# Kernel optimization log

Hardware: AMD Instinct MI355X
Metric: run time of the kernel (lower is better)

The kernel has to match this reference:

```python
import jax, jax.numpy as jnp
import numpy as np

B, S, H, D = 8, 1024, 16, 64  # batch, seq, heads, d_heads; hidden = H*D = 1024

def setup_inputs() -> dict:
    key = jax.random.key(0)
    ks = jax.random.split(key, 7)
    sc = 1.0 / np.sqrt(D)
    return {
        "sequences": jax.random.normal(ks[0], (B, S, H * D), dtype=jnp.float32),
        "Wq": jax.random.normal(ks[1], (H, D, D), dtype=jnp.float32) * sc,
        "bq": jax.random.normal(ks[2], (H, D), dtype=jnp.float32) * 0.01,
        "Wk": jax.random.normal(ks[3], (H, D, D), dtype=jnp.float32) * sc,
        "bk": jax.random.normal(ks[4], (H, D), dtype=jnp.float32) * 0.01,
        "Wv": jax.random.normal(ks[5], (H, D, D), dtype=jnp.float32) * sc,
        "bv": jax.random.normal(ks[6], (H, D), dtype=jnp.float32) * 0.01,
    }

def reference(sequences, Wq, bq, Wk, bk, Wv, bv):
    # sequences: [B, S, H*D] -> [B, S, H, D] (head h uses slice h*D:(h+1)*D)
    x = sequences.reshape(B, S, H, D)
    # per-head Linear: y = x @ W.T + b  (torch convention)
    q = jnp.einsum("bshd,hed->bshe", x, Wq) + bq
    k = jnp.einsum("bshd,hed->bshe", x, Wk) + bk
    v = jnp.einsum("bshd,hed->bshe", x, Wv) + bv
    scores = jnp.einsum("bqhd,bkhd->bhqk", q, k) / jnp.sqrt(jnp.float32(D))
    attn = jax.nn.softmax(scores, axis=-1)
    out = jnp.einsum("bhqk,bkhd->bqhd", attn, v)  # [B, S, H, D]
    return out.reshape(B, S, H * D)  # hstack over heads == reshape
```

## Files before the change

kernel.cpp:

```cpp
#include <hip/hip_runtime.h>
#include <hip/hip_bf16.h>


typedef __attribute__((ext_vector_type(8))) short short8;
typedef __attribute__((ext_vector_type(4))) float f32x4;
typedef __attribute__((ext_vector_type(16))) float f32x16;
typedef __attribute__((ext_vector_type(2))) unsigned int u32x2;
typedef __attribute__((ext_vector_type(4))) unsigned int u32x4;

#define MFMA16 __builtin_amdgcn_mfma_f32_16x16x32_bf16
#define MFMA32 __builtin_amdgcn_mfma_f32_32x32x16_bf16

#define QSCALE 0.1803368801111204f

__device__ __forceinline__ unsigned cvt_pk(float lo, float hi) {
  unsigned r;
  asm("v_cvt_pk_bf16_f32 %0, %1, %2" : "=v"(r) : "v"(lo), "v"(hi));
  return r;
}
__device__ __forceinline__ void pl32_swap(unsigned &a, unsigned &b) {
  asm("v_permlane32_swap_b32 %0, %1" : "+v"(a), "+v"(b));
}
__device__ __forceinline__ u32x2 pk4(const f32x4 v) {
  return (u32x2){cvt_pk(v[0], v[1]), cvt_pk(v[2], v[3])};
}
__device__ __forceinline__ void pack_cd(const f32x16& p, short8& lo, short8& hi8) {
  unsigned d0 = cvt_pk(p[0],  p[1]);
  unsigned d2 = cvt_pk(p[4],  p[5]);
  pl32_swap(d0, d2);
  unsigned d1 = cvt_pk(p[2],  p[3]);
  unsigned d3 = cvt_pk(p[6],  p[7]);
  pl32_swap(d1, d3);
  u32x4 a = {d0, d1, d2, d3};
  unsigned e0 = cvt_pk(p[8],  p[9]);
  unsigned e2 = cvt_pk(p[12], p[13]);
  pl32_swap(e0, e2);
  unsigned e1 = cvt_pk(p[10], p[11]);
  unsigned e3 = cvt_pk(p[14], p[15]);
  pl32_swap(e1, e3);
  u32x4 b = {e0, e1, e2, e3};
  lo  = __builtin_bit_cast(short8, a);
  hi8 = __builtin_bit_cast(short8, b);
}
__device__ __forceinline__ void lds_barrier() {
  asm volatile("s_waitcnt lgkmcnt(0)" ::: "memory");
  __builtin_amdgcn_s_barrier();
}

__global__ __launch_bounds__(256) void kv_proj_kernel(
    const float* __restrict__ x,
    const float* __restrict__ Wk, const float* __restrict__ bk,
    const float* __restrict__ Wv, const float* __restrict__ bv,
    unsigned short* __restrict__ kv_ws)
{
  __shared__ unsigned short x_lds[64][72];
  __shared__ unsigned short w_lds[2][64][72];

  const int h    = blockIdx.x & 15;
  const int tb   = blockIdx.x >> 4;
  const int tid  = threadIdx.x;
  const int lane = tid & 63;
  const int wv   = tid >> 6;
  const int g    = lane >> 4;
  const int cc   = lane & 15;

  {
    const int i  = tid >> 2;
    const int q4 = tid & 3;
    const float* xs  = x  + (size_t)(tb * 64 + i) * 1024 + h * 64 + q4 * 16;
    const float* wsk = Wk + (size_t)h * 4096 + i * 64 + q4 * 16;
    const float* wsv = Wv + (size_t)h * 4096 + i * 64 + q4 * 16;
#pragma unroll
    for (int it = 0; it < 4; ++it) {
      const int c = q4 * 16 + it * 4;
      *(u32x2*)&x_lds[i][c]    = pk4(*(const f32x4*)(xs  + it * 4));
      *(u32x2*)&w_lds[0][i][c] = pk4(*(const f32x4*)(wsk + it * 4));
      *(u32x2*)&w_lds[1][i][c] = pk4(*(const f32x4*)(wsv + it * 4));
    }
  }
  __syncthreads();

  f32x4 ak[4], av[4];
#pragma unroll
  for (int f = 0; f < 4; ++f) {
    ak[f] = (f32x4){0.f, 0.f, 0.f, 0.f};
    av[f] = (f32x4){0.f, 0.f, 0.f, 0.f};
  }

  const int arow = wv * 16 + cc;
  const int kc   = g * 8;
#pragma unroll
  for (int kk = 0; kk < 2; ++kk) {
    short8 a = *(const short8*)&x_lds[arow][kk * 32 + kc];
#pragma unroll
    for (int f = 0; f < 4; ++f) {
      const int br = f * 16 + cc;
      ak[f] = MFMA16(a, *(const short8*)&w_lds[0][br][kk * 32 + kc], ak[f], 0, 0, 0);
      av[f] = MFMA16(a, *(const short8*)&w_lds[1][br][kk * 32 + kc], av[f], 0, 0, 0);
    }
  }

  const int b   = tb >> 4;
  const int tk0 = wv * 16 + g * 4;
  unsigned short* kvt = kv_ws + (size_t)(b * 16 + h) * 131072
                              + (size_t)(tb & 15) * 8192;

  __syncthreads();
  unsigned short* Ak = &w_lds[0][0][0];
  unsigned short* Av = &x_lds[0][0];

#pragma unroll
  for (int f = 0; f < 4; ++f) {
    const int e = f * 16 + cc;
    const float bkv = bk[h * 64 + e];
    const float bvv = bv[h * 64 + e];
    u32x2 pkk;
    pkk[0] = cvt_pk(ak[f][0] + bkv, ak[f][1] + bkv);
    pkk[1] = cvt_pk(ak[f][2] + bkv, ak[f][3] + bkv);
    Ak[(tk0 + 0) * 72 + e] = (unsigned short)pkk[0];
    Ak[(tk0 + 1) * 72 + e] = (unsigned short)(pkk[0] >> 16);
    Ak[(tk0 + 2) * 72 + e] = (unsigned short)pkk[1];
    Ak[(tk0 + 3) * 72 + e] = (unsigned short)(pkk[1] >> 16);
    f32x4 vv;
#pragma unroll
    for (int r = 0; r < 4; ++r) vv[r] = av[f][r] + bvv;
    *(u32x2*)&Av[e * 72 + tk0] = pk4(vv);
  }
  __syncthreads();

#pragma unroll
  for (int half = 0; half < 2; ++half) {
    const int c   = tid + half * 256;
    const int oct = c >> 6;
    const int r2  = c & 63;
    const int slot = (oct >> 1) * 128 + (r2 >> 5) * 64 + (oct & 1) * 32 + (r2 & 31);
    short8 kcnk = *(const short8*)&Ak[r2 * 72 + oct * 8];
    *(short8*)&kvt[slot * 8] = kcnk;
    short8 vcnk = *(const short8*)&Av[r2 * 72 + oct * 8];
    *(short8*)&kvt[4096 + slot * 8] = vcnk;
  }
}

__global__ __launch_bounds__(512, 4) void attn_kernel(
    const float* __restrict__ x,
    const float* __restrict__ Wq, const float* __restrict__ bq,
    const unsigned short* __restrict__ kv_ws,
    float* __restrict__ out)
{
  __shared__ __align__(16) char lds[32768];

  const int logical = (blockIdx.x & 7) * 64 + (blockIdx.x >> 3);
  const int qt = logical & 3;
  const int bh = logical >> 2;
  const int b  = bh >> 4;
  const int h  = bh & 15;
  const unsigned short* kvb = kv_ws + (size_t)bh * 131072;

  const int tid = threadIdx.x;
  const int w   = tid >> 6;
  const int l   = tid & 63;
  const int hi  = l >> 5;
  const int cc  = l & 31;

  const unsigned short* sgp = kvb + tid * 8;
  char* wbp = lds + tid * 16;

  short8 st[2];
#pragma unroll
  for (int j = 0; j < 2; ++j) st[j] = *(const short8*)(sgp + j * 4096);

  unsigned short* wq_l = (unsigned short*)lds;
  unsigned short* xh_l = (unsigned short*)(lds + 9216);

  {
    const int r = tid >> 3, s = tid & 7;
    const float* ws = Wq + h * 4096 + r * 64 + s * 8;
    f32x4 v0 = *(const f32x4*)ws;
    f32x4 v1 = *(const f32x4*)(ws + 4);
    u32x4 d = {cvt_pk(v0[0], v0[1]), cvt_pk(v0[2], v0[3]),
               cvt_pk(v1[0], v1[1]), cvt_pk(v1[2], v1[3])};
    *(u32x4*)&wq_l[r * 72 + s * 8] = d;
  }

  short8 qf[4];
  f32x16 qa0 = {}, qa1 = {};
#pragma unroll
  for (int p = 0; p < 2; ++p) {
    {
      const int r = tid >> 2, s = tid & 3;
      const float* xs = x + ((size_t)(b * 1024 + qt * 256 + p * 128 + r)) * 1024
                          + h * 64 + s * 16;
      f32x4 v0 = *(const f32x4*)xs;
      f32x4 v1 = *(const f32x4*)(xs + 4);
      f32x4 v2 = *(const f32x4*)(xs + 8);
      f32x4 v3 = *(const f32x4*)(xs + 12);
      u32x4 d0 = {cvt_pk(v0[0], v0[1]), cvt_pk(v0[2], v0[3]),
                  cvt_pk(v1[0], v1[1]), cvt_pk(v1[2], v1[3])};
      u32x4 d1 = {cvt_pk(v2[0], v2[1]), cvt_pk(v2[2], v2[3]),
                  cvt_pk(v3[0], v3[1]), cvt_pk(v3[2], v3[3])};
      *(u32x4*)&xh_l[r * 72 + s * 16]     = d0;
      *(u32x4*)&xh_l[r * 72 + s * 16 + 8] = d1;
    }
    lds_barrier();
    if ((w >> 2) == p) {
      const int tl = (w & 3) * 32 + cc;
#pragma unroll
      for (int c = 0; c < 4; ++c) {
        short8 xf  = *(const short8*)&xh_l[tl * 72 + c * 16 + hi * 8];
        short8 alo = *(const short8*)&wq_l[cc * 72 + c * 16 + hi * 8];
        short8 ahi = *(const short8*)&wq_l[(32 + cc) * 72 + c * 16 + hi * 8];
        qa0 = MFMA32(alo, xf, qa0, 0, 0, 0);
        qa1 = MFMA32(ahi, xf, qa1, 0, 0, 0);
      }
    }
    lds_barrier();
  }
  {
#pragma unroll
    for (int r = 0; r < 16; ++r) {
      const int e = (r & 3) + 8 * (r >> 2) + 4 * hi;
      qa0[r] = (qa0[r] + bq[h * 64 + e]) * QSCALE;
      qa1[r] = (qa1[r] + bq[h * 64 + 32 + e]) * QSCALE;
    }
    pack_cd(qa0, qf[0], qf[1]);
    pack_cd(qa1, qf[2], qf[3]);
  }

#pragma unroll
  for (int j = 0; j < 2; ++j) *(short8*)(wbp + j * 8192) = st[j];
#pragma unroll
  for (int j = 0; j < 2; ++j) st[j] = *(const short8*)(sgp + 8192 + j * 4096);
  lds_barrier();

  f32x16 ot0 = {}; f32x16 ot1 = {};
  float lsum = 0.f;

  for (int kv = 0; kv < 16; ++kv) {
    if (kv < 15) {
      char* d = wbp + ((kv + 1) & 1) * 16384;
#pragma unroll
      for (int j = 0; j < 2; ++j) *(short8*)(d + j * 8192) = st[j];
      if (kv < 14) {
        const unsigned short* s = sgp + (size_t)(kv + 2) * 8192;
#pragma unroll
        for (int j = 0; j < 2; ++j) st[j] = *(const short8*)(s + j * 4096);
      }
    }
    const char* kb_ = lds + (kv & 1) * 16384;
    const char* vb_ = kb_ + 8192;

    f32x16 s0 = {}; f32x16 s1 = {};
    __builtin_amdgcn_s_setprio(1);
#pragma unroll
    for (int c = 0; c < 4; ++c) {
      s0 = MFMA32(*(const short8*)(kb_ + (c * 128 + l) * 16),      qf[c], s0, 0, 0, 0);
      s1 = MFMA32(*(const short8*)(kb_ + (c * 128 + 64 + l) * 16), qf[c], s1, 0, 0, 0);
    }
    __builtin_amdgcn_s_setprio(0);

    float ps0 = 0.f, ps1 = 0.f;
#pragma unroll
    for (int i = 0; i < 16; ++i) { s0[i] = __builtin_amdgcn_exp2f(s0[i]); ps0 += s0[i]; }
#pragma unroll
    for (int i = 0; i < 16; ++i) { s1[i] = __builtin_amdgcn_exp2f(s1[i]); ps1 += s1[i]; }
    lsum += ps0 + ps1;

#pragma unroll
    for (int kb = 0; kb < 2; ++kb) {
      short8 pa0, pa1;
      pack_cd(kb ? s1 : s0, pa0, pa1);

      const int c20 = kb * 2, c21 = kb * 2 + 1;
      __builtin_amdgcn_s_setprio(1);
      ot0 = MFMA32(*(const short8*)(vb_ + (c20 * 128 + l) * 16),      pa0, ot0, 0, 0, 0);
      ot1 = MFMA32(*(const short8*)(vb_ + (c20 * 128 + 64 + l) * 16), pa0, ot1, 0, 0, 0);
      ot0 = MFMA32(*(const short8*)(vb_ + (c21 * 128 + l) * 16),      pa1, ot0, 0, 0, 0);
      ot1 = MFMA32(*(const short8*)(vb_ + (c21 * 128 + 64 + l) * 16), pa1, ot1, 0, 0, 0);
      __builtin_amdgcn_s_setprio(0);
    }
    lds_barrier();
  }

  const float lt  = lsum + __shfl_xor(lsum, 32, 64);
  const float inv = 1.0f / lt;
  const int s_row = qt * 256 + w * 32 + cc;
  float* op = out + ((size_t)(b * 1024 + s_row) << 10) + h * 64;
#pragma unroll
  for (int rg = 0; rg < 4; ++rg) {
    const int d0 = 8 * rg + 4 * hi;
    f32x4 v0, v1;
#pragma unroll
    for (int j = 0; j < 4; ++j) {
      v0[j] = ot0[rg * 4 + j] * inv;
      v1[j] = ot1[rg * 4 + j] * inv;
    }
    *(f32x4*)(op + d0)      = v0;
    *(f32x4*)(op + 32 + d0) = v1;
  }
}

extern "C" void kernel_launch(void* const* d_in, const int* in_sizes, int n_in,
                              void* d_out, int out_size, void* d_ws, size_t ws_size,
                              hipStream_t stream) {
  const float* x  = (const float*)d_in[0];
  const float* Wq = (const float*)d_in[1];
  const float* bq = (const float*)d_in[2];
  const float* Wk = (const float*)d_in[3];
  const float* bk = (const float*)d_in[4];
  const float* Wv = (const float*)d_in[5];
  const float* bv = (const float*)d_in[6];
  float* out = (float*)d_out;

  unsigned short* kv_ws = (unsigned short*)d_ws;

  kv_proj_kernel<<<2048, 256, 0, stream>>>(x, Wk, bk, Wv, bv, kv_ws);
  attn_kernel<<<512, 512, 0, stream>>>(x, Wq, bq, kv_ws, out);
}
```

Baseline: 70.48 us.

## Compute K/V projection with 32x32 MFMA and write packed layout directly from registers

The K/V projection kernel switches from 16x16x32 MFMAs to 32x32x16 MFMAs. K is computed transposed (W times X) so the accumulator layout matches the attention kernel's expected chunk order. Results are packed with permlane-based pack_cd and stored straight to global memory, removing the LDS staging round-trip and two barriers. This relies on the register-to-slot mapping exactly matching the layout the attention kernel consumes.

Result: no change. 70.56 us (+0.1%).

```diff
diff --git a/kernel.cpp b/kernel.cpp
--- a/kernel.cpp
+++ b/kernel.cpp
@@ -56,13 +56,13 @@
   __shared__ unsigned short x_lds[64][72];
   __shared__ unsigned short w_lds[2][64][72];
 
-  const int h    = blockIdx.x & 15;
-  const int tb   = blockIdx.x >> 4;
-  const int tid  = threadIdx.x;
-  const int lane = tid & 63;
-  const int wv   = tid >> 6;
-  const int g    = lane >> 4;
-  const int cc   = lane & 15;
+  const int h   = blockIdx.x & 15;
+  const int tb  = blockIdx.x >> 4;
+  const int tid = threadIdx.x;
+  const int w   = tid >> 6;
+  const int l   = tid & 63;
+  const int hi  = l >> 5;
+  const int cc  = l & 31;
 
   {
     const int i  = tid >> 2;
@@ -80,64 +80,55 @@
   }
   __syncthreads();
 
-  f32x4 ak[4], av[4];
-#pragma unroll
-  for (int f = 0; f < 4; ++f) {
-    ak[f] = (f32x4){0.f, 0.f, 0.f, 0.f};
-    av[f] = (f32x4){0.f, 0.f, 0.f, 0.f};
-  }
-
-  const int arow = wv * 16 + cc;
-  const int kc   = g * 8;
-#pragma unroll
-  for (int kk = 0; kk < 2; ++kk) {
-    short8 a = *(const short8*)&x_lds[arow][kk * 32 + kc];
-#pragma unroll
-    for (int f = 0; f < 4; ++f) {
-      const int br = f * 16 + cc;
-      ak[f] = MFMA16(a, *(const short8*)&w_lds[0][br][kk * 32 + kc], ak[f], 0, 0, 0);
-      av[f] = MFMA16(a, *(const short8*)&w_lds[1][br][kk * 32 + kc], av[f], 0, 0, 0);
-    }
-  }
-
-  const int b   = tb >> 4;
-  const int tk0 = wv * 16 + g * 4;
+  const int b = tb >> 4;
   unsigned short* kvt = kv_ws + (size_t)(b * 16 + h) * 131072
                               + (size_t)(tb & 15) * 8192;
 
-  __syncthreads();
-  unsigned short* Ak = &w_lds[0][0][0];
-  unsigned short* Av = &x_lds[0][0];
-
-#pragma unroll
-  for (int f = 0; f < 4; ++f) {
-    const int e = f * 16 + cc;
-    const float bkv = bk[h * 64 + e];
-    const float bvv = bv[h * 64 + e];
-    u32x2 pkk;
-    pkk[0] = cvt_pk(ak[f][0] + bkv, ak[f][1] + bkv);
-    pkk[1] = cvt_pk(ak[f][2] + bkv, ak[f][3] + bkv);
-    Ak[(tk0 + 0) * 72 + e] = (unsigned short)pkk[0];
-    Ak[(tk0 + 1) * 72 + e] = (unsigned short)(pkk[0] >> 16);
-    Ak[(tk0 + 2) * 72 + e] = (unsigned short)pkk[1];
-    Ak[(tk0 + 3) * 72 + e] = (unsigned short)(pkk[1] >> 16);
-    f32x4 vv;
-#pragma unroll
-    for (int r = 0; r < 4; ++r) vv[r] = av[f][r] + bvv;
-    *(u32x2*)&Av[e * 72 + tk0] = pk4(vv);
-  }
-  __syncthreads();
-
-#pragma unroll
-  for (int half = 0; half < 2; ++half) {
-    const int c   = tid + half * 256;
-    const int oct = c >> 6;
-    const int r2  = c & 63;
-    const int slot = (oct >> 1) * 128 + (r2 >> 5) * 64 + (oct & 1) * 32 + (r2 & 31);
-    short8 kcnk = *(const short8*)&Ak[r2 * 72 + oct * 8];
-    *(short8*)&kvt[slot * 8] = kcnk;
-    short8 vcnk = *(const short8*)&Av[r2 * 72 + oct * 8];
-    *(short8*)&kvt[4096 + slot * 8] = vcnk;
+  {
+    const int eb = w >> 1, cb = w & 1;
+    f32x16 kkT = {};
+#pragma unroll
+    for (int ks = 0; ks < 4; ++ks) {
+      short8 aW = *(const short8*)&w_lds[0][eb * 32 + cc][ks * 16 + hi * 8];
+      short8 bX = *(const short8*)&x_lds[cb * 32 + cc][ks * 16 + hi * 8];
+      kkT = MFMA32(aW, bX, kkT, 0, 0, 0);
+    }
+    const float* bkb = bk + h * 64 + eb * 32 + 4 * hi;
+    f32x4 bk0 = *(const f32x4*)(bkb);
+    f32x4 bk1 = *(const f32x4*)(bkb + 8);
+    f32x4 bk2 = *(const f32x4*)(bkb + 16);
+    f32x4 bk3 = *(const f32x4*)(bkb + 24);
+#pragma unroll
+    for (int r = 0; r < 16; ++r) {
+      const float bb = (r >> 2) == 0 ? bk0[r & 3] :
+                       (r >> 2) == 1 ? bk1[r & 3] :
+                       (r >> 2) == 2 ? bk2[r & 3] : bk3[r & 3];
+      kkT[r] += bb;
+    }
+    short8 klo, khi;
+    pack_cd(kkT, klo, khi);
+    const int slot = 256 * eb + 64 * cb + 32 * hi + cc;
+    *(short8*)&kvt[slot * 8]         = klo;
+    *(short8*)&kvt[(slot + 128) * 8] = khi;
+  }
+
+  {
+    const int tb32 = w >> 1, db = w & 1;
+    f32x16 vvC = {};
+#pragma unroll
+    for (int ks = 0; ks < 4; ++ks) {
+      short8 aX = *(const short8*)&x_lds[tb32 * 32 + cc][ks * 16 + hi * 8];
+      short8 bW = *(const short8*)&w_lds[1][db * 32 + cc][ks * 16 + hi * 8];
+      vvC = MFMA32(aX, bW, vvC, 0, 0, 0);
+    }
+    const float bvv = bv[h * 64 + db * 32 + cc];
+#pragma unroll
+    for (int r = 0; r < 16; ++r) vvC[r] += bvv;
+    short8 vlo, vhi;
+    pack_cd(vvC, vlo, vhi);
+    const int slot = 256 * tb32 + 64 * db + 32 * hi + cc;
+    *(short8*)&kvt[4096 + slot * 8]         = vlo;
+    *(short8*)&kvt[4096 + (slot + 128) * 8] = vhi;
   }
 }
 
```
